# Kernel optimization log

Hardware: AMD Instinct MI355X
Metric: run time of the kernel (lower is better)

Reference implementation:

```python
import jax, jax.numpy as jnp
import numpy as np

T, B = 200, 256
X_DIM, H_DIM, Z_DIM, O_DIM = 128, 512, 64, 256


def setup_inputs() -> dict:
    key = jax.random.key(0)
    ks = iter(jax.random.split(key, 40))

    def lin_w(i, o):
        return (jax.random.normal(next(ks), (i, o), jnp.float32) / np.sqrt(i)).astype(jnp.float32)

    def lin_b(o):
        return jnp.zeros((o,), jnp.float32)

    inp = {
        "x": jax.random.normal(next(ks), (T, B, X_DIM), jnp.float32),
        "eps": jax.random.normal(next(ks), (T, B, Z_DIM), jnp.float32),
        # phi_x: Linear(x,h) ReLU Linear(h,h) ReLU
        "phi_x_w1": lin_w(X_DIM, H_DIM), "phi_x_b1": lin_b(H_DIM),
        "phi_x_w2": lin_w(H_DIM, H_DIM), "phi_x_b2": lin_b(H_DIM),
        # phi_z: Linear(z,h) ReLU
        "phi_z_w": lin_w(Z_DIM, H_DIM), "phi_z_b": lin_b(H_DIM),
        # enc: Linear(2h,h) ReLU Linear(h,h) ReLU
        "enc_w1": lin_w(2 * H_DIM, H_DIM), "enc_b1": lin_b(H_DIM),
        "enc_w2": lin_w(H_DIM, H_DIM), "enc_b2": lin_b(H_DIM),
        "enc_mean_w": lin_w(H_DIM, Z_DIM), "enc_mean_b": lin_b(Z_DIM),
        "enc_std_w": lin_w(H_DIM, Z_DIM), "enc_std_b": lin_b(Z_DIM),
        # prior: Linear(h,h) ReLU
        "prior_w": lin_w(H_DIM, H_DIM), "prior_b": lin_b(H_DIM),
        "prior_mean_w": lin_w(H_DIM, Z_DIM), "prior_mean_b": lin_b(Z_DIM),
        "prior_std_w": lin_w(H_DIM, Z_DIM), "prior_std_b": lin_b(Z_DIM),
        # dec: Linear(2h,h) ReLU Linear(h,h) ReLU
        "dec_w1": lin_w(2 * H_DIM, H_DIM), "dec_b1": lin_b(H_DIM),
        "dec_w2": lin_w(H_DIM, H_DIM), "dec_b2": lin_b(H_DIM),
        "dec_logits_w": lin_w(H_DIM, O_DIM), "dec_logits_b": lin_b(O_DIM),
        # GRU (1 layer): input 2h -> hidden h, gates ordered (r, z, n) as in torch
        "gru_w_ih": lin_w(2 * H_DIM, 3 * H_DIM), "gru_b_ih": lin_b(3 * H_DIM),
        "gru_w_hh": lin_w(H_DIM, 3 * H_DIM), "gru_b_hh": lin_b(3 * H_DIM),
    }
    return inp


def reference(x, eps, phi_x_w1, phi_x_b1, phi_x_w2, phi_x_b2, phi_z_w, phi_z_b,
              enc_w1, enc_b1, enc_w2, enc_b2, enc_mean_w, enc_mean_b, enc_std_w, enc_std_b,
              prior_w, prior_b, prior_mean_w, prior_mean_b, prior_std_w, prior_std_b,
              dec_w1, dec_b1, dec_w2, dec_b2, dec_logits_w, dec_logits_b,
              gru_w_ih, gru_w_hh, gru_b_ih, gru_b_hh):
    relu, sp, sig = jax.nn.relu, jax.nn.softplus, jax.nn.sigmoid
    # phi_x over all timesteps at once: [T, B, h]
    phi_x = relu(relu(x @ phi_x_w1 + phi_x_b1) @ phi_x_w2 + phi_x_b2)

    def step(h, inp):  # h: [B, h]
        px_t, eps_t = inp
        pr = relu(h @ prior_w + prior_b)
        pm = pr @ prior_mean_w + prior_mean_b
        ps = sp(pr @ prior_std_w + prior_std_b)
        e = jnp.concatenate([px_t, h], axis=1)
        e = relu(relu(e @ enc_w1 + enc_b1) @ enc_w2 + enc_b2)
        em = e @ enc_mean_w + enc_mean_b
        es = sp(e @ enc_std_w + enc_std_b)
        z_t = eps_t * es + em  # reparameterized sample
        pz = relu(z_t @ phi_z_w + phi_z_b)
        d = jnp.concatenate([pz, h], axis=1)
        d = relu(relu(d @ dec_w1 + dec_b1) @ dec_w2 + dec_b2)
        logits = d @ dec_logits_w + dec_logits_b
        # GRU cell (torch semantics, gate order r|z|n)
        gx = jnp.concatenate([px_t, pz], axis=1) @ gru_w_ih + gru_b_ih
        gh = h @ gru_w_hh + gru_b_hh
        xr, xz, xn = jnp.split(gx, 3, axis=1)
        hr, hz, hn = jnp.split(gh, 3, axis=1)
        r = sig(xr + hr)
        u = sig(xz + hz)
        n = jnp.tanh(xn + r * hn)
        h_new = (1.0 - u) * n + u * h
        kld = 0.5 * (2.0 * jnp.log(ps) - 2.0 * jnp.log(es)
                     + (es ** 2 + (em - pm) ** 2) / ps ** 2 - 1.0)
        return h_new, (z_t, logits, em, es, pm, ps, kld)

    h0 = jnp.zeros((x.shape[1], H_DIM), x.dtype)
    _, (z, o_logits, enc_mean, enc_std, prior_mean, prior_std, kld) = jax.lax.scan(
        step, h0, (phi_x, eps))
    return z, o_logits, enc_mean, enc_std, prior_mean, prior_std, kld
```

## Files before the change

kernel.cpp:

```cpp
#include <hip/hip_runtime.h>
#include <math.h>


#define TT 200
#define BB 256
#define HD 512
#define TB (TT*BB)

typedef unsigned short u16;
typedef _Float16 f16;
typedef __attribute__((ext_vector_type(8))) short bf16x8;
typedef __attribute__((ext_vector_type(4))) float f32x4;

constexpr size_t OFF_Z      = 0;
constexpr size_t OFF_LOGITS = 3276800;
constexpr size_t OFF_EM     = 16384000;
constexpr size_t OFF_ES     = 19660800;
constexpr size_t OFF_PM     = 22937600;
constexpr size_t OFF_PS     = 26214400;
constexpr size_t OFF_KLD    = 29491200;

__device__ __forceinline__ u16 f2bf(float f) {
  union { float f; unsigned u; } v; v.f = f;
  return (u16)((v.u + 0x7fffu + ((v.u >> 16) & 1u)) >> 16);
}
__device__ __forceinline__ float bf2f(u16 b) {
  union { unsigned u; float f; } v; v.u = ((unsigned)b) << 16; return v.f;
}
__device__ __forceinline__ float sp_(float x) { return (x > 15.f) ? x : log1pf(expf(x)); }
__device__ __forceinline__ float sigm_(float x) { return 1.f / (1.f + __expf(-x)); }
__device__ __forceinline__ float tanh_(float x) { return 1.f - 2.f / (1.f + __expf(2.f * x)); }

#define MFMA(a,b,c) __builtin_amdgcn_mfma_f32_16x16x32_bf16((a),(b),(c),0,0,0)

#define SWZ(row, cb)  (((row) << 10) + ((cb) ^ (((row) & 7) << 4)))
#define SWZZ(row, cb) (((row) << 7)  + ((cb) ^ (((row) & 7) << 4)))

#define NSEG 18
struct CastSeg { const float* src; u16* dst; int R; int C; };
struct CastArgs { CastSeg seg[NSEG]; };

__global__ __launch_bounds__(256) void cast_all(CastArgs a) {
  int idx = blockIdx.x * 256 + threadIdx.x;
  #pragma unroll 1
  for (int s = 0; s < NSEG; s++) {
    const int R = a.seg[s].R, C = a.seg[s].C;
    const int sz = R * C;
    if (idx < sz) {
      const int r = idx / C, c = idx - r * C;
      a.seg[s].dst[(size_t)c * R + r] = f2bf(a.seg[s].src[idx]);
      return;
    }
    idx -= sz;
  }
}

__global__ __launch_bounds__(256) void init_k(float* h_cur, u16* H0) {
  const int i = blockIdx.x * 256 + threadIdx.x;
  if (i < BB * HD) { h_cur[i] = 0.f; H0[i] = 0; }
}

struct GB {
  const void* A1; int lda1, K1, a1f32;
  const u16* Bt1;
  const u16* A2; int lda2, K2;
  const u16* Bt2;
  const float* bias;
  u16* outB; float* outF; f16* outH; int ldc;
  int tilesN; int act;
};

__device__ __forceinline__ bf16x8 load_a8(const void* A, int f32, size_t row, int lda, int k) {
  if (!f32) return *(const bf16x8*)((const u16*)A + row * (size_t)lda + k);
  const float* p = (const float*)A + row * (size_t)lda + k;
  f32x4 x0 = *(const f32x4*)p;
  f32x4 x1 = *(const f32x4*)(p + 4);
  bf16x8 r;
  r[0]=(short)f2bf(x0[0]); r[1]=(short)f2bf(x0[1]); r[2]=(short)f2bf(x0[2]); r[3]=(short)f2bf(x0[3]);
  r[4]=(short)f2bf(x1[0]); r[5]=(short)f2bf(x1[1]); r[6]=(short)f2bf(x1[2]); r[7]=(short)f2bf(x1[3]);
  return r;
}

__global__ __launch_bounds__(256) void gemm_bt(GB g) {
  const int tn = blockIdx.x % g.tilesN, tm = blockIdx.x / g.tilesN;
  const int m0 = tm * 64, n0 = tn * 64;
  const int v = threadIdx.x >> 6, l = threadIdx.x & 63, lm = l & 15, q = l >> 4;
  const size_t rowA = m0 + v * 16 + lm;
  f32x4 acc[4] = {};
  for (int k0 = 0; k0 < g.K1; k0 += 32) {
    bf16x8 a = load_a8(g.A1, g.a1f32, rowA, g.lda1, k0 + q * 8);
    #pragma unroll
    for (int c = 0; c < 4; c++) {
      bf16x8 b = *(const bf16x8*)(g.Bt1 + (size_t)(n0 + c * 16 + lm) * g.K1 + k0 + q * 8);
      acc[c] = MFMA(a, b, acc[c]);
    }
  }
  if (g.A2) {
    for (int k0 = 0; k0 < g.K2; k0 += 32) {
      bf16x8 a = *(const bf16x8*)(g.A2 + rowA * (size_t)g.lda2 + k0 + q * 8);
      #pragma unroll
      for (int c = 0; c < 4; c++) {
        bf16x8 b = *(const bf16x8*)(g.Bt2 + (size_t)(n0 + c * 16 + lm) * g.K2 + k0 + q * 8);
        acc[c] = MFMA(a, b, acc[c]);
      }
    }
  }
  #pragma unroll
  for (int c = 0; c < 4; c++) {
    const int col = n0 + c * 16 + lm;
    const float bs = g.bias ? g.bias[col] : 0.f;
    #pragma unroll
    for (int r = 0; r < 4; r++) {
      const size_t row = (size_t)m0 + v * 16 + q * 4 + r;
      float x = acc[c][r] + bs;
      if (g.act == 1) x = fmaxf(x, 0.f);
      if (g.outB) g.outB[row * g.ldc + col] = f2bf(x);
      if (g.outF) g.outF[row * g.ldc + col] = x;
      if (g.outH) g.outH[row * g.ldc + col] = (f16)x;
    }
  }
}

__global__ __launch_bounds__(256) void pms_kld(const u16* PR, const u16* pms_t,
                                               const float* pmb, const float* psb,
                                               float* out) {
  const int m0 = blockIdx.x * 64;
  const int v = threadIdx.x >> 6, l = threadIdx.x & 63, lm = l & 15, q = l >> 4;
  const size_t rowA = m0 + v * 16 + lm;
  f32x4 acc[8] = {};
  for (int k0 = 0; k0 < 512; k0 += 32) {
    bf16x8 a = *(const bf16x8*)(PR + rowA * 512 + k0 + q * 8);
    #pragma unroll
    for (int c = 0; c < 8; c++) {
      bf16x8 b = *(const bf16x8*)(pms_t + (size_t)(c * 16 + lm) * 512 + k0 + q * 8);
      acc[c] = MFMA(a, b, acc[c]);
    }
  }
  #pragma unroll
  for (int c = 0; c < 4; c++) {
    const int colz = c * 16 + lm;
    #pragma unroll
    for (int r = 0; r < 4; r++) {
      const size_t row = (size_t)m0 + v * 16 + q * 4 + r;
      const float pm = acc[c][r] + pmb[colz];
      const float ps = sp_(acc[c + 4][r] + psb[colz]);
      const size_t oi = row * 64 + colz;
      const float em = out[OFF_EM + oi], es = out[OFF_ES + oi];
      const float d = em - pm;
      const float kld = 0.5f * (2.f * logf(ps) - 2.f * logf(es)
                                + (es * es + d * d) / (ps * ps) - 1.f);
      out[OFF_PM + oi] = pm;
      out[OFF_PS + oi] = ps;
      out[OFF_KLD + oi] = kld;
    }
  }
}

struct SP {
  const u16 *pre_enc;
  u16 *pzbuf;
  u16 *H;
  float *h_cur;
  u16 *Abuf;
  float *GH;
  const f16 *gx;
  const u16 *enc_w1_h_t, *enc_w2_t, *ems_t, *phi_z_t, *gru_hh_t, *gru_ih_pz_t;
  const float *enc_b2, *enc_mean_b, *enc_std_b, *phi_z_b, *gru_b_hh;
  const float *eps;
  float *out;
};

__global__ __launch_bounds__(256) void ag_k(SP s, int t) {
  const int tn = blockIdx.x & 31, tm = blockIdx.x >> 5;
  const int v = threadIdx.x >> 6, l = threadIdx.x & 63, lm = l & 15, q = l >> 4;
  const int m0 = tm * 64;
  const size_t rowA = m0 + v * 16 + lm;
  const u16* Ht = s.H + (size_t)t * (BB * HD);
  const bool isA = (tn < 8);
  const int n0 = isA ? tn * 64 : (tn - 8) * 64;
  const u16* Bt = isA ? s.enc_w1_h_t : s.gru_hh_t;
  f32x4 acc[4] = {};
  for (int k0 = 0; k0 < 512; k0 += 32) {
    bf16x8 a = *(const bf16x8*)(Ht + rowA * 512 + k0 + q * 8);
    #pragma unroll
    for (int c = 0; c < 4; c++) {
      bf16x8 b = *(const bf16x8*)(Bt + (size_t)(n0 + c * 16 + lm) * 512 + k0 + q * 8);
      acc[c] = MFMA(a, b, acc[c]);
    }
  }
  if (isA) {
    const u16* pre = s.pre_enc + (size_t)t * (BB * HD);
    #pragma unroll
    for (int c = 0; c < 4; c++) {
      const int col = n0 + c * 16 + lm;
      #pragma unroll
      for (int r = 0; r < 4; r++) {
        const int row = m0 + v * 16 + q * 4 + r;
        const float x = acc[c][r] + bf2f(pre[(size_t)row * 512 + col]);
        s.Abuf[(size_t)row * 512 + col] = f2bf(fmaxf(x, 0.f));
      }
    }
  } else {
    #pragma unroll
    for (int c = 0; c < 4; c++) {
      const int colg = n0 + c * 16 + lm;
      const float bs = s.gru_b_hh[colg];
      #pragma unroll
      for (int r = 0; r < 4; r++) {
        const int row = m0 + v * 16 + q * 4 + r;
        s.GH[(size_t)row * 1536 + colg] = acc[c][r] + bs;
      }
    }
  }
}

__global__ __launch_bounds__(256) void et_k(SP s, int t) {
  const int w = blockIdx.x;
  const int tid = threadIdx.x;
  const int v = tid >> 6, l = tid & 63, lm = l & 15, q = l >> 4;
  const int r0 = w * 16;
  __shared__ u16 elds[16 * 512];
  __shared__ float emsb[16 * 128];
  __shared__ u16 zb[16 * 64];

  {
    f32x4 acc[8] = {};
    for (int k0 = 0; k0 < 512; k0 += 32) {
      bf16x8 a = *(const bf16x8*)(s.Abuf + (size_t)(r0 + lm) * 512 + k0 + q * 8);
      #pragma unroll
      for (int ct = 0; ct < 8; ct++) {
        bf16x8 b = *(const bf16x8*)(s.enc_w2_t + (size_t)(v * 128 + ct * 16 + lm) * 512 + k0 + q * 8);
        acc[ct] = MFMA(a, b, acc[ct]);
      }
    }
    #pragma unroll
    for (int ct = 0; ct < 8; ct++) {
      const int col = v * 128 + ct * 16 + lm;
      const float bs = s.enc_b2[col];
      #pragma unroll
      for (int r = 0; r < 4; r++) {
        const int row = q * 4 + r;
        *(u16*)((char*)elds + SWZ(row, col * 2)) = f2bf(fmaxf(acc[ct][r] + bs, 0.f));
      }
    }
  }
  __syncthreads();

  {
    f32x4 e0 = {}, e1 = {};
    const int cb = v * 32;
    for (int k0 = 0; k0 < 512; k0 += 32) {
      bf16x8 a  = *(const bf16x8*)((const char*)elds + SWZ(lm, (k0 + q * 8) * 2));
      bf16x8 b0 = *(const bf16x8*)(s.ems_t + (size_t)(cb + lm) * 512 + k0 + q * 8);
      bf16x8 b1 = *(const bf16x8*)(s.ems_t + (size_t)(cb + 16 + lm) * 512 + k0 + q * 8);
      e0 = MFMA(a, b0, e0);
      e1 = MFMA(a, b1, e1);
    }
    #pragma unroll
    for (int ct = 0; ct < 2; ct++) {
      const int col = cb + ct * 16 + lm;
      const float bs = (col < 64) ? s.enc_mean_b[col] : s.enc_std_b[col - 64];
      const f32x4 ee = ct ? e1 : e0;
      #pragma unroll
      for (int r = 0; r < 4; r++)
        emsb[(q * 4 + r) * 128 + col] = ee[r] + bs;
    }
  }
  __syncthreads();

  #pragma unroll
  for (int i = 0; i < 4; i++) {
    const int e = tid + i * 256;
    const int rr = e >> 6, cc = e & 63;
    const float em = emsb[rr * 128 + cc];
    const float es = sp_(emsb[rr * 128 + 64 + cc]);
    const int row = r0 + rr;
    const size_t oi = ((size_t)t * BB + row) * 64 + cc;
    const float z = s.eps[oi] * es + em;
    s.out[OFF_Z + oi]  = z;
    s.out[OFF_EM + oi] = em;
    s.out[OFF_ES + oi] = es;
    *(u16*)((char*)zb + SWZZ(rr, cc * 2)) = f2bf(z);
  }
  __syncthreads();

  {
    u16* pzg = s.pzbuf + (size_t)t * (BB * HD);
    #pragma unroll
    for (int ct = 0; ct < 8; ct++) {
      const int cz = v * 128 + ct * 16;
      f32x4 pa = {};
      #pragma unroll
      for (int k0 = 0; k0 < 64; k0 += 32) {
        bf16x8 a = *(const bf16x8*)((const char*)zb + SWZZ(lm, (k0 + q * 8) * 2));
        bf16x8 b = *(const bf16x8*)(s.phi_z_t + (size_t)(cz + lm) * 64 + k0 + q * 8);
        pa = MFMA(a, b, pa);
      }
      const int col = cz + lm;
      const float bs = s.phi_z_b[col];
      #pragma unroll
      for (int r = 0; r < 4; r++) {
        const int row = r0 + q * 4 + r;
        pzg[(size_t)row * 512 + col] = f2bf(fmaxf(pa[r] + bs, 0.f));
      }
    }
  }
}

__global__ __launch_bounds__(256) void gru_k(SP s, int t) {
  const int jt = blockIdx.x & 7, tm = blockIdx.x >> 3;
  const int v = threadIdx.x >> 6, l = threadIdx.x & 63, lm = l & 15, q = l >> 4;
  const int m0 = tm * 64, j0 = jt * 64;
  const size_t rowA = m0 + v * 16 + lm;
  const u16* pz = s.pzbuf + (size_t)t * (BB * HD);
  f32x4 acc[3][4] = {};
  for (int k0 = 0; k0 < 512; k0 += 32) {
    bf16x8 a = *(const bf16x8*)(pz + rowA * 512 + k0 + q * 8);
    #pragma unroll
    for (int g = 0; g < 3; g++) {
      #pragma unroll
      for (int c = 0; c < 4; c++) {
        bf16x8 b = *(const bf16x8*)(s.gru_ih_pz_t
                     + (size_t)(g * 512 + j0 + c * 16 + lm) * 512 + k0 + q * 8);
        acc[g][c] = MFMA(a, b, acc[g][c]);
      }
    }
  }
  const f16* gxt = s.gx + (size_t)t * BB * 1536;
  u16* Hn = s.H + (size_t)(t + 1) * (BB * HD);
  #pragma unroll
  for (int c = 0; c < 4; c++) {
    const int j = j0 + c * 16 + lm;
    #pragma unroll
    for (int r = 0; r < 4; r++) {
      const int row = m0 + v * 16 + q * 4 + r;
      const size_t base = (size_t)row * 1536;
      const float xr = acc[0][c][r] + (float)gxt[base + j];
      const float xz = acc[1][c][r] + (float)gxt[base + 512 + j];
      const float xn = acc[2][c][r] + (float)gxt[base + 1024 + j];
      const float hr = s.GH[base + j];
      const float hz = s.GH[base + 512 + j];
      const float hn = s.GH[base + 1024 + j];
      const float rg = sigm_(xr + hr);
      const float uu = sigm_(xz + hz);
      const float nn = tanh_(xn + rg * hn);
      const float hold = s.h_cur[(size_t)row * 512 + j];
      const float hnew = (1.f - uu) * nn + uu * hold;
      s.h_cur[(size_t)row * 512 + j] = hnew;
      Hn[(size_t)row * 512 + j] = f2bf(hnew);
    }
  }
}

extern "C" void kernel_launch(void* const* d_in, const int* in_sizes, int n_in,
                              void* d_out, int out_size, void* d_ws, size_t ws_size,
                              hipStream_t stream) {
  (void)in_sizes; (void)n_in; (void)out_size; (void)ws_size;
  char* ws = (char*)d_ws;
  float* out = (float*)d_out;
  auto in = [&](int i) { return (const float*)d_in[i]; };

  size_t o = 0;
  auto take = [&](size_t bytes) { size_t r = o; o += (bytes + 255) & ~(size_t)255; return r; };
  const size_t oPhiXW1  = take(512 * 128 * 2);
  const size_t oPhiXW2  = take(512 * 512 * 2);
  const size_t oEncW1px = take(512 * 512 * 2);
  const size_t oEncW1h  = take(512 * 512 * 2);
  const size_t oEncW2   = take(512 * 512 * 2);
  const size_t oEms     = take(128 * 512 * 2);
  const size_t oPhiZ    = take(512 * 64 * 2);
  const size_t oPriorW  = take(512 * 512 * 2);
  const size_t oPriorMs = take(128 * 512 * 2);
  const size_t oDecW1pz = take(512 * 512 * 2);
  const size_t oDecW1h  = take(512 * 512 * 2);
  const size_t oDecW2   = take(512 * 512 * 2);
  const size_t oDecLog  = take(256 * 512 * 2);
  const size_t oGruIhPx = take((size_t)1536 * 512 * 2);
  const size_t oGruIhPz = take((size_t)1536 * 512 * 2);
  const size_t oGruHh   = take((size_t)1536 * 512 * 2);
  const size_t oBuf0    = take((size_t)TB * 512 * 2);
  const size_t oBuf1    = take((size_t)TB * 512 * 2);
  const size_t oH       = take((size_t)(TT + 1) * BB * 512 * 2);
  const size_t oHcur    = take((size_t)BB * 512 * 4);
  const size_t oAbuf    = take((size_t)BB * 512 * 2);
  const size_t oGH      = take((size_t)BB * 1536 * 4);
  const size_t oGX      = take((size_t)TB * 1536 * 2);

  auto W = [&](size_t off) { return (u16*)(ws + off); };
  u16* BUF0 = W(oBuf0);
  u16* BUF1 = W(oBuf1);
  u16* Hbuf = W(oH);
  float* h_cur = (float*)(ws + oHcur);
  f16* GX16 = (f16*)(ws + oGX);

  CastArgs ca;
  int si = 0;
  auto seg = [&](const float* src, u16* dst, int R, int C) { ca.seg[si++] = {src, dst, R, C}; };
  seg(in(2), W(oPhiXW1), 128, 512);
  seg(in(4), W(oPhiXW2), 512, 512);
  seg(in(8), W(oEncW1px), 512, 512);
  seg(in(8) + 512 * 512, W(oEncW1h), 512, 512);
  seg(in(10), W(oEncW2), 512, 512);
  seg(in(12), W(oEms), 512, 64);
  seg(in(14), W(oEms) + 64 * 512, 512, 64);
  seg(in(6), W(oPhiZ), 64, 512);
  seg(in(16), W(oPriorW), 512, 512);
  seg(in(18), W(oPriorMs), 512, 64);
  seg(in(20), W(oPriorMs) + 64 * 512, 512, 64);
  seg(in(22), W(oDecW1pz), 512, 512);
  seg(in(22) + 512 * 512, W(oDecW1h), 512, 512);
  seg(in(24), W(oDecW2), 512, 512);
  seg(in(26), W(oDecLog), 512, 256);
  seg(in(28), W(oGruIhPx), 512, 1536);
  seg(in(28) + 512 * 1536, W(oGruIhPz), 512, 1536);
  seg(in(30), W(oGruHh), 512, 1536);
  hipLaunchKernelGGL(cast_all, dim3(18816), dim3(256), 0, stream, ca);
  hipLaunchKernelGGL(init_k, dim3(512), dim3(256), 0, stream, h_cur, Hbuf);

  auto gemm = [&](const void* A1, int lda1, int K1, int a1f32, const u16* Bt1,
                  const u16* A2, int lda2, int K2, const u16* Bt2,
                  const float* bias, u16* outB, float* outF, f16* outH,
                  int ldc, int N, int act) {
    GB g;
    g.A1 = A1; g.lda1 = lda1; g.K1 = K1; g.a1f32 = a1f32; g.Bt1 = Bt1;
    g.A2 = A2; g.lda2 = lda2; g.K2 = K2; g.Bt2 = Bt2;
    g.bias = bias; g.outB = outB; g.outF = outF; g.outH = outH; g.ldc = ldc;
    g.tilesN = N / 64; g.act = act;
    hipLaunchKernelGGL(gemm_bt, dim3((TB / 64) * (N / 64)), dim3(256), 0, stream, g);
  };

  gemm(in(0), 128, 128, 1, W(oPhiXW1), nullptr, 0, 0, nullptr, in(3), BUF0, nullptr, nullptr, 512, 512, 1);
  gemm(BUF0, 512, 512, 0, W(oPhiXW2), nullptr, 0, 0, nullptr, in(5), BUF1, nullptr, nullptr, 512, 512, 1);
  gemm(BUF1, 512, 512, 0, W(oEncW1px), nullptr, 0, 0, nullptr, in(9), BUF0, nullptr, nullptr, 512, 512, 0);
  gemm(BUF1, 512, 512, 0, W(oGruIhPx), nullptr, 0, 0, nullptr, in(29), nullptr, nullptr, GX16, 1536, 1536, 0);

  SP sp;
  sp.pre_enc = BUF0; sp.pzbuf = BUF0;
  sp.H = Hbuf; sp.h_cur = h_cur;
  sp.Abuf = W(oAbuf); sp.GH = (float*)(ws + oGH); sp.gx = GX16;
  sp.enc_w1_h_t = W(oEncW1h); sp.enc_w2_t = W(oEncW2); sp.ems_t = W(oEms);
  sp.phi_z_t = W(oPhiZ); sp.gru_hh_t = W(oGruHh); sp.gru_ih_pz_t = W(oGruIhPz);
  sp.enc_b2 = in(11); sp.enc_mean_b = in(13); sp.enc_std_b = in(15);
  sp.phi_z_b = in(7); sp.gru_b_hh = in(31);
  sp.eps = in(1); sp.out = out;
  for (int t = 0; t < TT; t++) {
    hipLaunchKernelGGL(ag_k,  dim3(128), dim3(256), 0, stream, sp, t);
    hipLaunchKernelGGL(et_k,  dim3(16),  dim3(256), 0, stream, sp, t);
    hipLaunchKernelGGL(gru_k, dim3(32),  dim3(256), 0, stream, sp, t);
  }

  gemm(Hbuf, 512, 512, 0, W(oPriorW), nullptr, 0, 0, nullptr, in(17), BUF1, nullptr, nullptr, 512, 512, 1);
  hipLaunchKernelGGL(pms_kld, dim3(TB / 64), dim3(256), 0, stream,
                     BUF1, W(oPriorMs), in(19), in(21), out);
  gemm(BUF0, 512, 512, 0, W(oDecW1pz), Hbuf, 512, 512, W(oDecW1h), in(23), BUF1, nullptr, nullptr, 512, 512, 1);
  gemm(BUF1, 512, 512, 0, W(oDecW2), nullptr, 0, 0, nullptr, in(25), BUF0, nullptr, nullptr, 512, 512, 1);
  gemm(BUF0, 512, 512, 0, W(oDecLog), nullptr, 0, 0, nullptr, in(27), nullptr, out + OFF_LOGITS, nullptr, 256, 256, 0);
}
```

Before: 18.52 ms.

## Split encoder layer-2 into parallel GEMM and fuse z sampling with GRU input gates

The per-step encoder second-layer GEMM moves out of the 16-block et_k kernel into a 32-block launch of the generic gemm_bt kernel, raising parallelism on that serial-path matmul. The mean/std projection, z sampling, phi_z and the GRU input-gate GEMM plus gate math are fused into one 32-block kernel. Each block recomputes mean/std and phi_z for its 64 rows in LDS, which removes the global round trip of pz before the GRU. The cost is redundant recomputation across the 8 column tiles, larger LDS use, and 32 accumulator tiles per thread that may pressure registers.

Result: slower. 20.88 ms (+12.7%).

```diff
diff --git a/kernel.cpp b/kernel.cpp
--- a/kernel.cpp
+++ b/kernel.cpp
@@ -162,10 +162,11 @@
   u16 *H;
   float *h_cur;
   u16 *Abuf;
+  u16 *Ebuf;
   float *GH;
   const f16 *gx;
-  const u16 *enc_w1_h_t, *enc_w2_t, *ems_t, *phi_z_t, *gru_hh_t, *gru_ih_pz_t;
-  const float *enc_b2, *enc_mean_b, *enc_std_b, *phi_z_b, *gru_b_hh;
+  const u16 *enc_w1_h_t, *ems_t, *phi_z_t, *gru_hh_t, *gru_ih_pz_t;
+  const float *enc_mean_b, *enc_std_b, *phi_z_b, *gru_b_hh;
   const float *eps;
   float *out;
 };
@@ -214,140 +215,126 @@
   }
 }
 
-__global__ __launch_bounds__(256) void et_k(SP s, int t) {
-  const int w = blockIdx.x;
+__global__ __launch_bounds__(256) void zg_k(SP s, int t) {
+  const int jt = blockIdx.x & 7, tm = blockIdx.x >> 3;
   const int tid = threadIdx.x;
   const int v = tid >> 6, l = tid & 63, lm = l & 15, q = l >> 4;
-  const int r0 = w * 16;
-  __shared__ u16 elds[16 * 512];
-  __shared__ float emsb[16 * 128];
-  __shared__ u16 zb[16 * 64];
+  const int m0 = tm * 64, j0 = jt * 64;
+
+  __shared__ float emsb[64 * 128];
+  __shared__ u16 zb[64 * 64];
+  __shared__ u16 pzl[64 * 512];
 
   {
-    f32x4 acc[8] = {};
+    const int cb = v * 32;
+    f32x4 acc[4][2] = {};
     for (int k0 = 0; k0 < 512; k0 += 32) {
-      bf16x8 a = *(const bf16x8*)(s.Abuf + (size_t)(r0 + lm) * 512 + k0 + q * 8);
-      #pragma unroll
-      for (int ct = 0; ct < 8; ct++) {
-        bf16x8 b = *(const bf16x8*)(s.enc_w2_t + (size_t)(v * 128 + ct * 16 + lm) * 512 + k0 + q * 8);
-        acc[ct] = MFMA(a, b, acc[ct]);
-      }
-    }
-    #pragma unroll
-    for (int ct = 0; ct < 8; ct++) {
-      const int col = v * 128 + ct * 16 + lm;
-      const float bs = s.enc_b2[col];
-      #pragma unroll
-      for (int r = 0; r < 4; r++) {
-        const int row = q * 4 + r;
-        *(u16*)((char*)elds + SWZ(row, col * 2)) = f2bf(fmaxf(acc[ct][r] + bs, 0.f));
-      }
-    }
-  }
-  __syncthreads();
-
-  {
-    f32x4 e0 = {}, e1 = {};
-    const int cb = v * 32;
-    for (int k0 = 0; k0 < 512; k0 += 32) {
-      bf16x8 a  = *(const bf16x8*)((const char*)elds + SWZ(lm, (k0 + q * 8) * 2));
       bf16x8 b0 = *(const bf16x8*)(s.ems_t + (size_t)(cb + lm) * 512 + k0 + q * 8);
       bf16x8 b1 = *(const bf16x8*)(s.ems_t + (size_t)(cb + 16 + lm) * 512 + k0 + q * 8);
-      e0 = MFMA(a, b0, e0);
-      e1 = MFMA(a, b1, e1);
+      #pragma unroll
+      for (int mt = 0; mt < 4; mt++) {
+        bf16x8 a = *(const bf16x8*)(s.Ebuf + (size_t)(m0 + mt * 16 + lm) * 512 + k0 + q * 8);
+        acc[mt][0] = MFMA(a, b0, acc[mt][0]);
+        acc[mt][1] = MFMA(a, b1, acc[mt][1]);
+      }
     }
     #pragma unroll
     for (int ct = 0; ct < 2; ct++) {
       const int col = cb + ct * 16 + lm;
       const float bs = (col < 64) ? s.enc_mean_b[col] : s.enc_std_b[col - 64];
-      const f32x4 ee = ct ? e1 : e0;
-      #pragma unroll
-      for (int r = 0; r < 4; r++)
-        emsb[(q * 4 + r) * 128 + col] = ee[r] + bs;
+      #pragma unroll
+      for (int mt = 0; mt < 4; mt++)
+        #pragma unroll
+        for (int r = 0; r < 4; r++)
+          emsb[(mt * 16 + q * 4 + r) * 128 + col] = acc[mt][ct][r] + bs;
     }
   }
   __syncthreads();
 
   #pragma unroll
-  for (int i = 0; i < 4; i++) {
+  for (int i = 0; i < 16; i++) {
     const int e = tid + i * 256;
     const int rr = e >> 6, cc = e & 63;
     const float em = emsb[rr * 128 + cc];
     const float es = sp_(emsb[rr * 128 + 64 + cc]);
-    const int row = r0 + rr;
+    const int row = m0 + rr;
     const size_t oi = ((size_t)t * BB + row) * 64 + cc;
     const float z = s.eps[oi] * es + em;
-    s.out[OFF_Z + oi]  = z;
-    s.out[OFF_EM + oi] = em;
-    s.out[OFF_ES + oi] = es;
+    if (jt == 0) {
+      s.out[OFF_Z + oi]  = z;
+      s.out[OFF_EM + oi] = em;
+      s.out[OFF_ES + oi] = es;
+    }
     *(u16*)((char*)zb + SWZZ(rr, cc * 2)) = f2bf(z);
   }
   __syncthreads();
 
   {
+    f32x4 pa[32];
+    #pragma unroll
+    for (int n = 0; n < 32; n++) pa[n] = (f32x4){0.f, 0.f, 0.f, 0.f};
+    #pragma unroll
+    for (int k0 = 0; k0 < 64; k0 += 32) {
+      bf16x8 a = *(const bf16x8*)((const char*)zb + SWZZ(v * 16 + lm, (k0 + q * 8) * 2));
+      #pragma unroll
+      for (int n = 0; n < 32; n++) {
+        bf16x8 b = *(const bf16x8*)(s.phi_z_t + (size_t)(n * 16 + lm) * 64 + k0 + q * 8);
+        pa[n] = MFMA(a, b, pa[n]);
+      }
+    }
     u16* pzg = s.pzbuf + (size_t)t * (BB * HD);
     #pragma unroll
-    for (int ct = 0; ct < 8; ct++) {
-      const int cz = v * 128 + ct * 16;
-      f32x4 pa = {};
-      #pragma unroll
-      for (int k0 = 0; k0 < 64; k0 += 32) {
-        bf16x8 a = *(const bf16x8*)((const char*)zb + SWZZ(lm, (k0 + q * 8) * 2));
-        bf16x8 b = *(const bf16x8*)(s.phi_z_t + (size_t)(cz + lm) * 64 + k0 + q * 8);
-        pa = MFMA(a, b, pa);
-      }
-      const int col = cz + lm;
+    for (int n = 0; n < 32; n++) {
+      const int col = n * 16 + lm;
       const float bs = s.phi_z_b[col];
       #pragma unroll
       for (int r = 0; r < 4; r++) {
-        const int row = r0 + q * 4 + r;
-        pzg[(size_t)row * 512 + col] = f2bf(fmaxf(pa[r] + bs, 0.f));
-      }
-    }
-  }
-}
-
-__global__ __launch_bounds__(256) void gru_k(SP s, int t) {
-  const int jt = blockIdx.x & 7, tm = blockIdx.x >> 3;
-  const int v = threadIdx.x >> 6, l = threadIdx.x & 63, lm = l & 15, q = l >> 4;
-  const int m0 = tm * 64, j0 = jt * 64;
-  const size_t rowA = m0 + v * 16 + lm;
-  const u16* pz = s.pzbuf + (size_t)t * (BB * HD);
-  f32x4 acc[3][4] = {};
-  for (int k0 = 0; k0 < 512; k0 += 32) {
-    bf16x8 a = *(const bf16x8*)(pz + rowA * 512 + k0 + q * 8);
-    #pragma unroll
-    for (int g = 0; g < 3; g++) {
-      #pragma unroll
-      for (int c = 0; c < 4; c++) {
-        bf16x8 b = *(const bf16x8*)(s.gru_ih_pz_t
-                     + (size_t)(g * 512 + j0 + c * 16 + lm) * 512 + k0 + q * 8);
-        acc[g][c] = MFMA(a, b, acc[g][c]);
-      }
-    }
-  }
-  const f16* gxt = s.gx + (size_t)t * BB * 1536;
-  u16* Hn = s.H + (size_t)(t + 1) * (BB * HD);
-  #pragma unroll
-  for (int c = 0; c < 4; c++) {
-    const int j = j0 + c * 16 + lm;
-    #pragma unroll
-    for (int r = 0; r < 4; r++) {
-      const int row = m0 + v * 16 + q * 4 + r;
-      const size_t base = (size_t)row * 1536;
-      const float xr = acc[0][c][r] + (float)gxt[base + j];
-      const float xz = acc[1][c][r] + (float)gxt[base + 512 + j];
-      const float xn = acc[2][c][r] + (float)gxt[base + 1024 + j];
-      const float hr = s.GH[base + j];
-      const float hz = s.GH[base + 512 + j];
-      const float hn = s.GH[base + 1024 + j];
-      const float rg = sigm_(xr + hr);
-      const float uu = sigm_(xz + hz);
-      const float nn = tanh_(xn + rg * hn);
-      const float hold = s.h_cur[(size_t)row * 512 + j];
-      const float hnew = (1.f - uu) * nn + uu * hold;
-      s.h_cur[(size_t)row * 512 + j] = hnew;
-      Hn[(size_t)row * 512 + j] = f2bf(hnew);
+        const int rloc = v * 16 + q * 4 + r;
+        const u16 val = f2bf(fmaxf(pa[n][r] + bs, 0.f));
+        *(u16*)((char*)pzl + SWZ(rloc, col * 2)) = val;
+        if (jt == 0) pzg[(size_t)(m0 + rloc) * 512 + col] = val;
+      }
+    }
+  }
+  __syncthreads();
+
+  {
+    f32x4 acc[3][4] = {};
+    for (int k0 = 0; k0 < 512; k0 += 32) {
+      bf16x8 a = *(const bf16x8*)((const char*)pzl + SWZ(v * 16 + lm, (k0 + q * 8) * 2));
+      #pragma unroll
+      for (int g = 0; g < 3; g++) {
+        #pragma unroll
+        for (int c = 0; c < 4; c++) {
+          bf16x8 b = *(const bf16x8*)(s.gru_ih_pz_t
+                       + (size_t)(g * 512 + j0 + c * 16 + lm) * 512 + k0 + q * 8);
+          acc[g][c] = MFMA(a, b, acc[g][c]);
+        }
+      }
+    }
+    const f16* gxt = s.gx + (size_t)t * BB * 1536;
+    u16* Hn = s.H + (size_t)(t + 1) * (BB * HD);
+    #pragma unroll
+    for (int c = 0; c < 4; c++) {
+      const int j = j0 + c * 16 + lm;
+      #pragma unroll
+      for (int r = 0; r < 4; r++) {
+        const int row = m0 + v * 16 + q * 4 + r;
+        const size_t base = (size_t)row * 1536;
+        const float xr = acc[0][c][r] + (float)gxt[base + j];
+        const float xz = acc[1][c][r] + (float)gxt[base + 512 + j];
+        const float xn = acc[2][c][r] + (float)gxt[base + 1024 + j];
+        const float hr = s.GH[base + j];
+        const float hz = s.GH[base + 512 + j];
+        const float hn = s.GH[base + 1024 + j];
+        const float rg = sigm_(xr + hr);
+        const float uu = sigm_(xz + hz);
+        const float nn = tanh_(xn + rg * hn);
+        const float hold = s.h_cur[(size_t)row * 512 + j];
+        const float hnew = (1.f - uu) * nn + uu * hold;
+        s.h_cur[(size_t)row * 512 + j] = hnew;
+        Hn[(size_t)row * 512 + j] = f2bf(hnew);
+      }
     }
   }
 }
@@ -383,6 +370,7 @@
   const size_t oH       = take((size_t)(TT + 1) * BB * 512 * 2);
   const size_t oHcur    = take((size_t)BB * 512 * 4);
   const size_t oAbuf    = take((size_t)BB * 512 * 2);
+  const size_t oEbuf    = take((size_t)BB * 512 * 2);
   const size_t oGH      = take((size_t)BB * 1536 * 4);
   const size_t oGX      = take((size_t)TB * 1536 * 2);
 
@@ -420,39 +408,47 @@
   auto gemm = [&](const void* A1, int lda1, int K1, int a1f32, const u16* Bt1,
                   const u16* A2, int lda2, int K2, const u16* Bt2,
                   const float* bias, u16* outB, float* outF, f16* outH,
-                  int ldc, int N, int act) {
+                  int ldc, int M, int N, int act) {
     GB g;
     g.A1 = A1; g.lda1 = lda1; g.K1 = K1; g.a1f32 = a1f32; g.Bt1 = Bt1;
     g.A2 = A2; g.lda2 = lda2; g.K2 = K2; g.Bt2 = Bt2;
     g.bias = bias; g.outB = outB; g.outF = outF; g.outH = outH; g.ldc = ldc;
     g.tilesN = N / 64; g.act = act;
-    hipLaunchKernelGGL(gemm_bt, dim3((TB / 64) * (N / 64)), dim3(256), 0, stream, g);
+    hipLaunchKernelGGL(gemm_bt, dim3((M / 64) * (N / 64)), dim3(256), 0, stream, g);
   };
 
-  gemm(in(0), 128, 128, 1, W(oPhiXW1), nullptr, 0, 0, nullptr, in(3), BUF0, nullptr, nullptr, 512, 512, 1);
-  gemm(BUF0, 512, 512, 0, W(oPhiXW2), nullptr, 0, 0, nullptr, in(5), BUF1, nullptr, nullptr, 512, 512, 1);
-  gemm(BUF1, 512, 512, 0, W(oEncW1px), nullptr, 0, 0, nullptr, in(9), BUF0, nullptr, nullptr, 512, 512, 0);
-  gemm(BUF1, 512, 512, 0, W(oGruIhPx), nullptr, 0, 0, nullptr, in(29), nullptr, nullptr, GX16, 1536, 1536, 0);
+  gemm(in(0), 128, 128, 1, W(oPhiXW1), nullptr, 0, 0, nullptr, in(3), BUF0, nullptr, nullptr, 512, TB, 512, 1);
+  gemm(BUF0, 512, 512, 0, W(oPhiXW2), nullptr, 0, 0, nullptr, in(5), BUF1, nullptr, nullptr, 512, TB, 512, 1);
+  gemm(BUF1, 512, 512, 0, W(oEncW1px), nullptr, 0, 0, nullptr, in(9), BUF0, nullptr, nullptr, 512, TB, 512, 0);
+  gemm(BUF1, 512, 512, 0, W(oGruIhPx), nullptr, 0, 0, nullptr, in(29), nullptr, nullptr, GX16, 1536, TB, 1536, 0);
 
   SP sp;
   sp.pre_enc = BUF0; sp.pzbuf = BUF0;
   sp.H = Hbuf; sp.h_cur = h_cur;
-  sp.Abuf = W(oAbuf); sp.GH = (float*)(ws + oGH); sp.gx = GX16;
-  sp.enc_w1_h_t = W(oEncW1h); sp.enc_w2_t = W(oEncW2); sp.ems_t = W(oEms);
+  sp.Abuf = W(oAbuf); sp.Ebuf = W(oEbuf);
+  sp.GH = (float*)(ws + oGH); sp.gx = GX16;
+  sp.enc_w1_h_t = W(oEncW1h); sp.ems_t = W(oEms);
   sp.phi_z_t = W(oPhiZ); sp.gru_hh_t = W(oGruHh); sp.gru_ih_pz_t = W(oGruIhPz);
-  sp.enc_b2 = in(11); sp.enc_mean_b = in(13); sp.enc_std_b = in(15);
+  sp.enc_mean_b = in(13); sp.enc_std_b = in(15);
   sp.phi_z_b = in(7); sp.gru_b_hh = in(31);
   sp.eps = in(1); sp.out = out;
+
+  GB ge;
+  ge.A1 = W(oAbuf); ge.lda1 = 512; ge.K1 = 512; ge.a1f32 = 0; ge.Bt1 = W(oEncW2);
+  ge.A2 = nullptr; ge.lda2 = 0; ge.K2 = 0; ge.Bt2 = nullptr;
+  ge.bias = in(11); ge.outB = W(oEbuf); ge.outF = nullptr; ge.outH = nullptr;
+  ge.ldc = 512; ge.tilesN = 8; ge.act = 1;
+
   for (int t = 0; t < TT; t++) {
-    hipLaunchKernelGGL(ag_k,  dim3(128), dim3(256), 0, stream, sp, t);
-    hipLaunchKernelGGL(et_k,  dim3(16),  dim3(256), 0, stream, sp, t);
-    hipLaunchKernelGGL(gru_k, dim3(32),  dim3(256), 0, stream, sp, t);
-  }
-
-  gemm(Hbuf, 512, 512, 0, W(oPriorW), nullptr, 0, 0, nullptr, in(17), BUF1, nullptr, nullptr, 512, 512, 1);
+    hipLaunchKernelGGL(ag_k,    dim3(128), dim3(256), 0, stream, sp, t);
+    hipLaunchKernelGGL(gemm_bt, dim3(32),  dim3(256), 0, stream, ge);
+    hipLaunchKernelGGL(zg_k,    dim3(32),  dim3(256), 0, stream, sp, t);
+  }
+
+  gemm(Hbuf, 512, 512, 0, W(oPriorW), nullptr, 0, 0, nullptr, in(17), BUF1, nullptr, nullptr, 512, TB, 512, 1);
   hipLaunchKernelGGL(pms_kld, dim3(TB / 64), dim3(256), 0, stream,
                      BUF1, W(oPriorMs), in(19), in(21), out);
-  gemm(BUF0, 512, 512, 0, W(oDecW1pz), Hbuf, 512, 512, W(oDecW1h), in(23), BUF1, nullptr, nullptr, 512, 512, 1);
-  gemm(BUF1, 512, 512, 0, W(oDecW2), nullptr, 0, 0, nullptr, in(25), BUF0, nullptr, nullptr, 512, 512, 1);
-  gemm(BUF0, 512, 512, 0, W(oDecLog), nullptr, 0, 0, nullptr, in(27), nullptr, out + OFF_LOGITS, nullptr, 256, 256, 0);
-}
+  gemm(BUF0, 512, 512, 0, W(oDecW1pz), Hbuf, 512, 512, W(oDecW1h), in(23), BUF1, nullptr, nullptr, 512, TB, 512, 1);
+  gemm(BUF1, 512, 512, 0, W(oDecW2), nullptr, 0, 0, nullptr, in(25), BUF0, nullptr, nullptr, 512, TB, 512, 1);
+  gemm(BUF0, 512, 512, 0, W(oDecLog), nullptr, 0, 0, nullptr, in(27), nullptr, out + OFF_LOGITS, nullptr, 256, TB, 256, 0);
+}
```
